# Optimization experiments

Hardware: AMD Instinct MI355X
Metric: run time of the kernel (lower is better)

## Reference

```python
import jax, jax.numpy as jnp
import numpy as np

S, B, H = 2048, 32, 1024

def setup_inputs() -> dict:
    key = jax.random.key(0)
    ks = jax.random.split(key, 8)
    return {
        "hidden": jax.random.normal(ks[0], (1, B, H), dtype=jnp.float32),
        "hidden_sequence": jax.random.normal(ks[1], (S, B, H), dtype=jnp.float32),
        "input_masks": jax.random.bernoulli(ks[2], 0.5, (S, B)),
        "W1": jax.random.normal(ks[3], (H, H), dtype=jnp.float32) * 0.02,
        "b1": jax.random.normal(ks[4], (H,), dtype=jnp.float32) * 0.02,
        "W2": jax.random.normal(ks[5], (H, H), dtype=jnp.float32) * 0.02,
        "b2": jax.random.normal(ks[6], (H,), dtype=jnp.float32) * 0.02,
        "v": jax.random.uniform(ks[7], (H,), dtype=jnp.float32),
    }

def reference(hidden, hidden_sequence, input_masks, W1, b1, W2, b2, v):
    # hidden: (1,B,H) broadcast over S; hidden_sequence: (S,B,H)
    # additive (Bahdanau) energy: v . tanh(W1 hs + W2 h)  -> (S,B)
    pre = (jnp.einsum('sbh,kh->sbk', hidden_sequence, W1) + b1
           + jnp.einsum('obh,kh->obk', hidden, W2) + b2)  # (S,B,H)
    energy = jnp.einsum('sbh,h->sb', jnp.tanh(pre), v)     # (S,B)
    energy = jnp.where(input_masks, energy, jnp.float32(-1e10))
    attn = jax.nn.softmax(energy, axis=0)                  # softmax over seq per batch
    context = jnp.einsum('sb,sbh->bh', attn, hidden_sequence)[None]  # (1,B,H)
    return context
```

## Files before the change

kernel.cpp:

```cpp
#include <hip/hip_runtime.h>
#include <stdint.h>


#define SS 2048
#define BB 32
#define HH 1024
#define MM (SS*BB)

typedef _Float16 f16;
typedef __attribute__((ext_vector_type(8))) _Float16 f16x8;
typedef __attribute__((ext_vector_type(4))) _Float16 f16x4;
typedef __attribute__((ext_vector_type(4))) float   floatx4;

__device__ __forceinline__ float tanh_fast(float x) {
  float e = __expf(2.0f * x);
  return 1.0f - 2.0f / (e + 1.0f);
}

__device__ __forceinline__ void gload16(void* lds_base, const void* gptr) {
  __builtin_amdgcn_global_load_lds(
      (const __attribute__((address_space(1))) uint32_t*)(uintptr_t)gptr,
      (__attribute__((address_space(3))) uint32_t*)(uint32_t)(uintptr_t)lds_base,
      16, 0, 0);
}

__global__ __launch_bounds__(256) void convert_f16(
    const float* __restrict__ hs, const float* __restrict__ W1,
    f16* __restrict__ hsf, f16* __restrict__ W1f)
{
  const size_t NH = (size_t)MM * HH;
  size_t base = ((size_t)blockIdx.x * 256 + threadIdx.x) * 8;
  if (base < NH) {
    floatx4 a = *(const floatx4*)&hs[base];
    floatx4 b = *(const floatx4*)&hs[base + 4];
    f16x8 o = {(f16)a.x,(f16)a.y,(f16)a.z,(f16)a.w,(f16)b.x,(f16)b.y,(f16)b.z,(f16)b.w};
    *(f16x8*)&hsf[base] = o;
  } else {
    size_t wb = base - NH;
    if (wb < (size_t)HH * HH) {
      floatx4 a = *(const floatx4*)&W1[wb];
      floatx4 b = *(const floatx4*)&W1[wb + 4];
      f16x8 o = {(f16)a.x,(f16)a.y,(f16)a.z,(f16)a.w,(f16)b.x,(f16)b.y,(f16)b.z,(f16)b.w};
      *(f16x8*)&W1f[wb] = o;
    }
  }
}

__global__ __launch_bounds__(256) void t2_kernel(
    const float* __restrict__ hidden, const float* __restrict__ W2,
    const float* __restrict__ b1, const float* __restrict__ b2,
    float* __restrict__ t2)
{
  const int gw   = blockIdx.x * 4 + (threadIdx.x >> 6);
  const int n    = gw >> 5;
  const int b    = gw & 31;
  const int lane = threadIdx.x & 63;
  float acc = 0.f;
#pragma unroll
  for (int q = 0; q < 4; ++q) {
    floatx4 hv = *(const floatx4*)&hidden[b * HH + q * 256 + lane * 4];
    floatx4 wv = *(const floatx4*)&W2[(size_t)n * HH + q * 256 + lane * 4];
    acc += hv.x * wv.x + hv.y * wv.y + hv.z * wv.z + hv.w * wv.w;
  }
#pragma unroll
  for (int off = 1; off < 64; off <<= 1) acc += __shfl_xor(acc, off);
  if (lane == 0) t2[b * HH + n] = acc + b1[n] + b2[n];
}

__global__ __launch_bounds__(256) void gemm_energy_f16(
    const f16* __restrict__ hsf, const f16* __restrict__ W1f,
    const float* __restrict__ t2, const float* __restrict__ v,
    float* __restrict__ epart)
{
  __shared__ __align__(16) f16 Asm[128 * 64];
  __shared__ __align__(16) f16 Bsm[128 * 64];

  const int tid  = threadIdx.x;
  const int lane = tid & 63;
  const int w    = tid >> 6;
  const int quad = lane >> 4;
  const int l15  = lane & 15;
  const int wr   = w >> 1, wc = w & 1;

  const int l     = blockIdx.x;
  const int x     = l & 7;
  const int jj_   = l >> 3;
  const int nb    = jj_ & 7;
  const int mtile = (jj_ >> 3) * 8 + x;
  const int mB    = mtile * 128;
  const int nB    = nb * 128;

  floatx4 acc[4][4];
#pragma unroll
  for (int i = 0; i < 4; ++i)
#pragma unroll
    for (int j = 0; j < 4; ++j) acc[i][j] = (floatx4){0.f, 0.f, 0.f, 0.f};

  for (int kt = 0; kt < HH; kt += 64) {
#pragma unroll
    for (int q = 0; q < 4; ++q) {
      const int W   = w * 4 + q;
      const int r   = W * 8 + (lane >> 3);
      const int cbl = (lane & 7) ^ (r & 7);
      gload16(&Asm[W * 64 * 8], &hsf[(size_t)(mB + r) * HH + kt + cbl * 8]);
      gload16(&Bsm[W * 64 * 8], &W1f[(size_t)(nB + r) * HH + kt + cbl * 8]);
    }
    __syncthreads();
#pragma unroll
    for (int ks = 0; ks < 2; ++ks) {
      f16x8 af[4], bfr[4];
#pragma unroll
      for (int i = 0; i < 4; ++i) {
        const int r   = wr * 64 + i * 16 + l15;
        const int cbp = (ks * 4 + quad) ^ (r & 7);
        af[i] = *(const f16x8*)&Asm[(r * 8 + cbp) * 8];
      }
#pragma unroll
      for (int j = 0; j < 4; ++j) {
        const int r   = wc * 64 + j * 16 + l15;
        const int cbp = (ks * 4 + quad) ^ (r & 7);
        bfr[j] = *(const f16x8*)&Bsm[(r * 8 + cbp) * 8];
      }
#pragma unroll
      for (int i = 0; i < 4; ++i)
#pragma unroll
        for (int j = 0; j < 4; ++j)
          acc[i][j] = __builtin_amdgcn_mfma_f32_16x16x32_f16(af[i], bfr[j], acc[i][j], 0, 0, 0);
    }
    __syncthreads();
  }

  float vv[4];
#pragma unroll
  for (int j = 0; j < 4; ++j) vv[j] = v[nB + wc * 64 + j * 16 + l15];
#pragma unroll
  for (int i = 0; i < 4; ++i) {
#pragma unroll
    for (int reg = 0; reg < 4; ++reg) {
      const int m = mB + wr * 64 + i * 16 + quad * 4 + reg;
      const int b = m & (BB - 1);
      float rs = 0.f;
#pragma unroll
      for (int j = 0; j < 4; ++j) {
        const int n = nB + wc * 64 + j * 16 + l15;
        rs += tanh_fast(acc[i][j][reg] + t2[b * HH + n]) * vv[j];
      }
      rs += __shfl_xor(rs, 1);
      rs += __shfl_xor(rs, 2);
      rs += __shfl_xor(rs, 4);
      rs += __shfl_xor(rs, 8);
      if (l15 == 0) epart[(size_t)(nb * 2 + wc) * MM + m] = rs;
    }
  }
}

__global__ __launch_bounds__(256) void softmax16(
    const float* __restrict__ epart, const int* __restrict__ masks,
    float* __restrict__ attn)
{
  const int b = blockIdx.x;
  const int tid = threadIdx.x;
  __shared__ float redm[4], reds[4];
  float em[8];
  float lmax = -3e38f;
#pragma unroll
  for (int it = 0; it < 8; ++it) {
    const int s = it * 256 + tid;
    float e = 0.f;
#pragma unroll
    for (int p = 0; p < 16; ++p) e += epart[(size_t)p * MM + s * BB + b];
    if (masks[s * BB + b] == 0) e = -1e10f;
    em[it] = e;
    lmax = fmaxf(lmax, e);
  }
#pragma unroll
  for (int off = 1; off < 64; off <<= 1) lmax = fmaxf(lmax, __shfl_xor(lmax, off));
  if ((tid & 63) == 0) redm[tid >> 6] = lmax;
  __syncthreads();
  lmax = fmaxf(fmaxf(redm[0], redm[1]), fmaxf(redm[2], redm[3]));
  float lsum = 0.f;
#pragma unroll
  for (int it = 0; it < 8; ++it) { em[it] = __expf(em[it] - lmax); lsum += em[it]; }
#pragma unroll
  for (int off = 1; off < 64; off <<= 1) lsum += __shfl_xor(lsum, off);
  if ((tid & 63) == 0) reds[tid >> 6] = lsum;
  __syncthreads();
  const float inv = 1.0f / (reds[0] + reds[1] + reds[2] + reds[3]);
#pragma unroll
  for (int it = 0; it < 8; ++it) attn[(it * 256 + tid) * BB + b] = em[it] * inv;
}

__global__ __launch_bounds__(256) void context_f16(
    const f16* __restrict__ hsf, const float* __restrict__ attn,
    float* __restrict__ ctxp)
{
  const int b  = blockIdx.x;
  const int sc = blockIdx.y;
  const int tid = threadIdx.x;
  floatx4 acc = {0.f, 0.f, 0.f, 0.f};
  for (int s = sc * 64; s < sc * 64 + 64; ++s) {
    const float a = attn[s * BB + b];
    if (a != 0.f) {
      f16x4 h = *(const f16x4*)&hsf[(size_t)(s * BB + b) * HH + tid * 4];
      acc.x += a * (float)h[0];
      acc.y += a * (float)h[1];
      acc.z += a * (float)h[2];
      acc.w += a * (float)h[3];
    }
  }
  *(floatx4*)&ctxp[(size_t)(sc * BB + b) * HH + tid * 4] = acc;
}

__global__ __launch_bounds__(256) void ctx_reduce32(
    const float* __restrict__ ctxp, float* __restrict__ out)
{
  const int i = blockIdx.x * 256 + threadIdx.x;
  float s = 0.f;
#pragma unroll
  for (int sc = 0; sc < 32; ++sc) s += ctxp[(size_t)sc * (BB * HH) + i];
  out[i] = s;
}

__global__ __launch_bounds__(256) void gemm_energy_fb(
    const float* __restrict__ hs, const float* __restrict__ W1,
    const float* __restrict__ t2, const float* __restrict__ v,
    float* __restrict__ epart)
{
  const int tid = threadIdx.x;
  const int nb  = blockIdx.x;
  const int mB  = blockIdx.y * 128;
  __shared__ __align__(16) f16 Asm[128][72];
  __shared__ __align__(16) f16 Bsm[128][72];
  const int lane = tid & 63;
  const int w    = tid >> 6;
  const int quad = lane >> 4;
  const int l15  = lane & 15;
  floatx4 acc[2][8];
#pragma unroll
  for (int i = 0; i < 2; ++i)
#pragma unroll
    for (int j = 0; j < 8; ++j) acc[i][j] = (floatx4){0.f, 0.f, 0.f, 0.f};
  const int srow = tid >> 4;
  const int scol = (tid & 15) * 4;
  const float* Abase = hs + (size_t)(mB + srow) * HH + scol;
  const float* Bbase = W1 + (size_t)(nb * 128 + srow) * HH + scol;
  for (int kt = 0; kt < HH; kt += 64) {
#pragma unroll
    for (int p = 0; p < 8; ++p) {
      floatx4 fa = *(const floatx4*)(Abase + (size_t)(p * 16) * HH + kt);
      floatx4 fb = *(const floatx4*)(Bbase + (size_t)(p * 16) * HH + kt);
      f16x4 ha = {(f16)fa.x, (f16)fa.y, (f16)fa.z, (f16)fa.w};
      f16x4 hb = {(f16)fb.x, (f16)fb.y, (f16)fb.z, (f16)fb.w};
      *(f16x4*)&Asm[p * 16 + srow][scol] = ha;
      *(f16x4*)&Bsm[p * 16 + srow][scol] = hb;
    }
    __syncthreads();
#pragma unroll
    for (int ks = 0; ks < 2; ++ks) {
      f16x8 af[2], bfr[8];
#pragma unroll
      for (int i = 0; i < 2; ++i)
        af[i] = *(const f16x8*)&Asm[w * 32 + i * 16 + l15][ks * 32 + quad * 8];
#pragma unroll
      for (int j = 0; j < 8; ++j)
        bfr[j] = *(const f16x8*)&Bsm[j * 16 + l15][ks * 32 + quad * 8];
#pragma unroll
      for (int i = 0; i < 2; ++i)
#pragma unroll
        for (int j = 0; j < 8; ++j)
          acc[i][j] = __builtin_amdgcn_mfma_f32_16x16x32_f16(af[i], bfr[j], acc[i][j], 0, 0, 0);
    }
    __syncthreads();
  }
  const int nB = nb * 128;
#pragma unroll
  for (int i = 0; i < 2; ++i) {
#pragma unroll
    for (int reg = 0; reg < 4; ++reg) {
      const int m = mB + w * 32 + i * 16 + quad * 4 + reg;
      const int b = m & (BB - 1);
      float rs = 0.f;
#pragma unroll
      for (int j = 0; j < 8; ++j) {
        const int n = nB + j * 16 + l15;
        rs += tanh_fast(acc[i][j][reg] + t2[b * HH + n]) * v[n];
      }
      rs += __shfl_xor(rs, 1);
      rs += __shfl_xor(rs, 2);
      rs += __shfl_xor(rs, 4);
      rs += __shfl_xor(rs, 8);
      if (l15 == 0) epart[(size_t)nb * MM + m] = rs;
    }
  }
}

__global__ __launch_bounds__(256) void softmax8(
    const float* __restrict__ epart, const int* __restrict__ masks,
    float* __restrict__ attn)
{
  const int b = blockIdx.x;
  const int tid = threadIdx.x;
  __shared__ float redm[4], reds[4];
  float em[8];
  float lmax = -3e38f;
#pragma unroll
  for (int it = 0; it < 8; ++it) {
    const int s = it * 256 + tid;
    float e = 0.f;
#pragma unroll
    for (int p = 0; p < 8; ++p) e += epart[(size_t)p * MM + s * BB + b];
    if (masks[s * BB + b] == 0) e = -1e10f;
    em[it] = e;
    lmax = fmaxf(lmax, e);
  }
#pragma unroll
  for (int off = 1; off < 64; off <<= 1) lmax = fmaxf(lmax, __shfl_xor(lmax, off));
  if ((tid & 63) == 0) redm[tid >> 6] = lmax;
  __syncthreads();
  lmax = fmaxf(fmaxf(redm[0], redm[1]), fmaxf(redm[2], redm[3]));
  float lsum = 0.f;
#pragma unroll
  for (int it = 0; it < 8; ++it) { em[it] = __expf(em[it] - lmax); lsum += em[it]; }
#pragma unroll
  for (int off = 1; off < 64; off <<= 1) lsum += __shfl_xor(lsum, off);
  if ((tid & 63) == 0) reds[tid >> 6] = lsum;
  __syncthreads();
  const float inv = 1.0f / (reds[0] + reds[1] + reds[2] + reds[3]);
#pragma unroll
  for (int it = 0; it < 8; ++it) attn[(it * 256 + tid) * BB + b] = em[it] * inv;
}

__global__ __launch_bounds__(256) void context_fb(
    const float* __restrict__ hs, const float* __restrict__ attn,
    float* __restrict__ ctxp)
{
  const int b  = blockIdx.x;
  const int sc = blockIdx.y;
  const int tid = threadIdx.x;
  floatx4 acc = {0.f, 0.f, 0.f, 0.f};
  for (int s = sc * 256; s < sc * 256 + 256; ++s) {
    const float a = attn[s * BB + b];
    if (a != 0.f) {
      floatx4 h = *(const floatx4*)&hs[(size_t)(s * BB + b) * HH + tid * 4];
      acc.x += a * h.x; acc.y += a * h.y; acc.z += a * h.z; acc.w += a * h.w;
    }
  }
  *(floatx4*)&ctxp[(size_t)(sc * BB + b) * HH + tid * 4] = acc;
}

__global__ __launch_bounds__(256) void ctx_reduce8(
    const float* __restrict__ ctxp, float* __restrict__ out)
{
  const int i = blockIdx.x * 256 + threadIdx.x;
  float s = 0.f;
#pragma unroll
  for (int sc = 0; sc < 8; ++sc) s += ctxp[(size_t)sc * (BB * HH) + i];
  out[i] = s;
}

extern "C" void kernel_launch(void* const* d_in, const int* in_sizes, int n_in,
                              void* d_out, int out_size, void* d_ws, size_t ws_size,
                              hipStream_t stream) {
  const float* hidden = (const float*)d_in[0];
  const float* hs     = (const float*)d_in[1];
  const int*   masks  = (const int*)d_in[2];
  const float* W1     = (const float*)d_in[3];
  const float* b1     = (const float*)d_in[4];
  const float* W2     = (const float*)d_in[5];
  const float* b2     = (const float*)d_in[6];
  const float* v      = (const float*)d_in[7];
  float* out = (float*)d_out;

  const size_t hsf_b   = (size_t)MM * HH * 2;
  const size_t w1f_b   = (size_t)HH * HH * 2;
  const size_t epart_b = (size_t)16 * MM * 4;
  const size_t attn_b  = (size_t)MM * 4;
  const size_t t2_b    = (size_t)BB * HH * 4;
  const size_t ctxp_b  = (size_t)32 * BB * HH * 4;
  const size_t need = hsf_b + w1f_b + epart_b + attn_b + t2_b + ctxp_b;

  if (ws_size >= need) {
    char* p = (char*)d_ws;
    f16*   hsf   = (f16*)p;              p += hsf_b;
    f16*   W1f   = (f16*)p;              p += w1f_b;
    float* epart = (float*)p;            p += epart_b;
    float* attn  = (float*)p;            p += attn_b;
    float* t2    = (float*)p;            p += t2_b;
    float* ctxp  = (float*)p;

    convert_f16<<<dim3(33280), 256, 0, stream>>>(hs, W1, hsf, W1f);
    t2_kernel<<<dim3(BB * HH / 4), 256, 0, stream>>>(hidden, W2, b1, b2, t2);
    gemm_energy_f16<<<dim3(4096), 256, 0, stream>>>(hsf, W1f, t2, v, epart);
    softmax16<<<dim3(BB), 256, 0, stream>>>(epart, masks, attn);
    context_f16<<<dim3(BB, 32), 256, 0, stream>>>(hsf, attn, ctxp);
    ctx_reduce32<<<dim3(BB * HH / 256), 256, 0, stream>>>(ctxp, out);
  } else {
    float* epart = (float*)d_ws;
    float* attn  = epart + 8 * MM;
    float* t2    = attn + MM;
    float* ctxp  = t2 + BB * HH;

    t2_kernel<<<dim3(BB * HH / 4), 256, 0, stream>>>(hidden, W2, b1, b2, t2);
    gemm_energy_fb<<<dim3(8, MM / 128), 256, 0, stream>>>(hs, W1, t2, v, epart);
    softmax8<<<dim3(BB), 256, 0, stream>>>(epart, masks, attn);
    context_fb<<<dim3(BB, 8), 256, 0, stream>>>(hs, attn, ctxp);
    ctx_reduce8<<<dim3(BB * HH / 256), 256, 0, stream>>>(ctxp, out);
  }
}
```

Baseline: 710.2 us.

## Transpose energy and attention buffers to batch-major, widen softmax blocks

The partial energies and attention weights are now stored batch-major (b*S+s) instead of seq-major. The softmax then reads contiguous, coalesced memory per batch, and it runs with 1024 threads per block instead of 256. The context kernel stages its 64 attention weights in shared memory and partially unrolls its loop. The GEMM epilogue stores become strided scalar writes, which may cost some write coalescing.

```diff
diff --git a/kernel.cpp b/kernel.cpp
--- a/kernel.cpp
+++ b/kernel.cpp
@@ -139,6 +139,7 @@
     for (int reg = 0; reg < 4; ++reg) {
       const int m = mB + wr * 64 + i * 16 + quad * 4 + reg;
       const int b = m & (BB - 1);
+      const int s = m >> 5;
       float rs = 0.f;
 #pragma unroll
       for (int j = 0; j < 4; ++j) {
@@ -149,26 +150,26 @@
       rs += __shfl_xor(rs, 2);
       rs += __shfl_xor(rs, 4);
       rs += __shfl_xor(rs, 8);
-      if (l15 == 0) epart[(size_t)(nb * 2 + wc) * MM + m] = rs;
-    }
-  }
-}
-
-__global__ __launch_bounds__(256) void softmax16(
+      if (l15 == 0) epart[(size_t)(nb * 2 + wc) * MM + b * SS + s] = rs;
+    }
+  }
+}
+
+__global__ __launch_bounds__(1024) void softmax16t(
     const float* __restrict__ epart, const int* __restrict__ masks,
     float* __restrict__ attn)
 {
   const int b = blockIdx.x;
   const int tid = threadIdx.x;
-  __shared__ float redm[4], reds[4];
-  float em[8];
+  __shared__ float redm[16], reds[16];
+  float em[2];
   float lmax = -3e38f;
 #pragma unroll
-  for (int it = 0; it < 8; ++it) {
-    const int s = it * 256 + tid;
+  for (int it = 0; it < 2; ++it) {
+    const int s = it * 1024 + tid;
     float e = 0.f;
 #pragma unroll
-    for (int p = 0; p < 16; ++p) e += epart[(size_t)p * MM + s * BB + b];
+    for (int p = 0; p < 16; ++p) e += epart[(size_t)p * MM + b * SS + s];
     if (masks[s * BB + b] == 0) e = -1e10f;
     em[it] = e;
     lmax = fmaxf(lmax, e);
@@ -177,31 +178,39 @@
   for (int off = 1; off < 64; off <<= 1) lmax = fmaxf(lmax, __shfl_xor(lmax, off));
   if ((tid & 63) == 0) redm[tid >> 6] = lmax;
   __syncthreads();
-  lmax = fmaxf(fmaxf(redm[0], redm[1]), fmaxf(redm[2], redm[3]));
+#pragma unroll
+  for (int i = 0; i < 16; ++i) lmax = fmaxf(lmax, redm[i]);
   float lsum = 0.f;
 #pragma unroll
-  for (int it = 0; it < 8; ++it) { em[it] = __expf(em[it] - lmax); lsum += em[it]; }
+  for (int it = 0; it < 2; ++it) { em[it] = __expf(em[it] - lmax); lsum += em[it]; }
 #pragma unroll
   for (int off = 1; off < 64; off <<= 1) lsum += __shfl_xor(lsum, off);
   if ((tid & 63) == 0) reds[tid >> 6] = lsum;
   __syncthreads();
-  const float inv = 1.0f / (reds[0] + reds[1] + reds[2] + reds[3]);
-#pragma unroll
-  for (int it = 0; it < 8; ++it) attn[(it * 256 + tid) * BB + b] = em[it] * inv;
-}
-
-__global__ __launch_bounds__(256) void context_f16(
+  float tsum = 0.f;
+#pragma unroll
+  for (int i = 0; i < 16; ++i) tsum += reds[i];
+  const float inv = 1.0f / tsum;
+#pragma unroll
+  for (int it = 0; it < 2; ++it) attn[b * SS + it * 1024 + tid] = em[it] * inv;
+}
+
+__global__ __launch_bounds__(256) void context_f16t(
     const f16* __restrict__ hsf, const float* __restrict__ attn,
     float* __restrict__ ctxp)
 {
   const int b  = blockIdx.x;
   const int sc = blockIdx.y;
   const int tid = threadIdx.x;
+  __shared__ float sat[64];
+  if (tid < 64) sat[tid] = attn[b * SS + sc * 64 + tid];
+  __syncthreads();
   floatx4 acc = {0.f, 0.f, 0.f, 0.f};
-  for (int s = sc * 64; s < sc * 64 + 64; ++s) {
-    const float a = attn[s * BB + b];
+#pragma unroll 4
+  for (int s = 0; s < 64; ++s) {
+    const float a = sat[s];
     if (a != 0.f) {
-      f16x4 h = *(const f16x4*)&hsf[(size_t)(s * BB + b) * HH + tid * 4];
+      f16x4 h = *(const f16x4*)&hsf[(size_t)((sc * 64 + s) * BB + b) * HH + tid * 4];
       acc.x += a * (float)h[0];
       acc.y += a * (float)h[1];
       acc.z += a * (float)h[2];
@@ -391,8 +400,8 @@
     convert_f16<<<dim3(33280), 256, 0, stream>>>(hs, W1, hsf, W1f);
     t2_kernel<<<dim3(BB * HH / 4), 256, 0, stream>>>(hidden, W2, b1, b2, t2);
     gemm_energy_f16<<<dim3(4096), 256, 0, stream>>>(hsf, W1f, t2, v, epart);
-    softmax16<<<dim3(BB), 256, 0, stream>>>(epart, masks, attn);
-    context_f16<<<dim3(BB, 32), 256, 0, stream>>>(hsf, attn, ctxp);
+    softmax16t<<<dim3(BB), 1024, 0, stream>>>(epart, masks, attn);
+    context_f16t<<<dim3(BB, 32), 256, 0, stream>>>(hsf, attn, ctxp);
     ctx_reduce32<<<dim3(BB * HH / 256), 256, 0, stream>>>(ctxp, out);
   } else {
     float* epart = (float*)d_ws;
```

New measurement: 650.1 us. 1.09x faster.
